# Performance work log

Hardware: AMD Instinct MI355X
Metric: run time of the kernel (lower is better)

Reference implementation:

```python
import jax, jax.numpy as jnp
import numpy as np
from jax import lax

B, S, E, DF, H, L, V, T = 32, 512, 512, 2048, 8, 2, 30000, 12
START, STOP = 10, 11
NEG = -10000.0


def setup_inputs() -> dict:
    key = jax.random.key(0)
    ks = jax.random.split(key, 12)
    g = lambda i, shape, sc=0.02: jax.random.normal(ks[i], shape, jnp.float32) * sc
    trans = jax.random.normal(ks[9], (T, T), jnp.float32)
    trans = trans.at[START, :].set(NEG).at[:, STOP].set(NEG)
    return {
        "sentence": jax.random.randint(ks[0], (B, S), 0, V),
        "seq_len": jax.random.randint(ks[1], (B,), 1, S + 1),
        "tags": jax.random.randint(ks[2], (B, S), 0, 10),
        "emb": g(3, (V, E), 1.0),
        "attn_in_w": g(4, (L, 3 * E, E)), "attn_in_b": jnp.zeros((L, 3 * E)),
        "attn_out_w": g(5, (L, E, E)), "attn_out_b": jnp.zeros((L, E)),
        "ln1_g": jnp.ones((L, E)), "ln1_b": jnp.zeros((L, E)),
        "ln2_g": jnp.ones((L, E)), "ln2_b": jnp.zeros((L, E)),
        "ff1_w": g(6, (L, DF, E)), "ff1_b": jnp.zeros((L, DF)),
        "ff2_w": g(7, (L, E, DF)), "ff2_b": jnp.zeros((L, E)),
        "tag_w": g(8, (T, E)), "tag_b": jnp.zeros((T,)),
        "transitions": trans,
    }


def _ln(x, g, b):
    m = x.mean(-1, keepdims=True)
    v = ((x - m) ** 2).mean(-1, keepdims=True)
    return (x - m) / jnp.sqrt(v + 1e-5) * g + b


def _mha(x, w_in, b_in, w_out, b_out):
    b_, s_, e_ = x.shape
    d = e_ // H
    qkv = x @ w_in.T + b_in
    q, k, v = jnp.split(qkv, 3, axis=-1)
    split = lambda t: t.reshape(b_, s_, H, d).transpose(0, 2, 1, 3)
    q, k, v = split(q), split(k), split(v)
    att = jax.nn.softmax(jnp.einsum('bhqd,bhkd->bhqk', q, k) / np.sqrt(d).astype(np.float32), axis=-1)
    o = jnp.einsum('bhqk,bhkd->bhqd', att, v).transpose(0, 2, 1, 3).reshape(b_, s_, e_)
    return o @ w_out.T + b_out


def _forward_impl(sentence, seq_len, tags, emb, attn_in_w, attn_in_b, attn_out_w,
                  attn_out_b, ln1_g, ln1_b, ln2_g, ln2_b, ff1_w, ff1_b, ff2_w,
                  ff2_b, tag_w, tag_b, transitions):
    # Transformer encoder features (dropout in eval mode -> identity)
    x = emb[sentence]  # (B,S,E)
    for l in range(L):
        x = _ln(x + _mha(x, attn_in_w[l], attn_in_b[l], attn_out_w[l], attn_out_b[l]), ln1_g[l], ln1_b[l])
        h = jax.nn.relu(x @ ff1_w[l].T + ff1_b[l]) @ ff2_w[l].T + ff2_b[l]
        x = _ln(x + h, ln2_g[l], ln2_b[l])
    feats = x @ tag_w.T + tag_b  # (B,S,T)

    # CRF forward algorithm (log-semiring scan, masked by seq_len)
    alpha0 = jnp.full((B, T), NEG, feats.dtype).at[:, START].set(0.0)

    def step(alpha, xs):
        emit_t, t = xs  # emit_t: (B,T)
        new = emit_t + jax.nn.logsumexp(alpha[:, None, :] + transitions[None, :, :], axis=-1)
        return jnp.where((t < seq_len)[:, None], new, alpha), None

    alpha, _ = lax.scan(step, alpha0, (feats.transpose(1, 0, 2), jnp.arange(S)))
    fwd_score = jax.nn.logsumexp(alpha + transitions[STOP][None, :], axis=-1)  # (B,)

    # gold score (vectorized _score_sentence)
    tags_ext = jnp.concatenate([jnp.full((B, 1), START, tags.dtype), tags], axis=1)  # (B,S+1)
    mask = jnp.arange(S)[None, :] < seq_len[:, None]  # (B,S)
    trans_sc = jnp.where(mask, transitions[tags_ext[:, 1:], tags_ext[:, :-1]], 0.0).sum(-1)
    emit_sc = jnp.where(mask, jnp.take_along_axis(feats, tags[:, :, None], axis=2)[..., 0], 0.0).sum(-1)
    last_tag = jnp.take_along_axis(tags_ext, seq_len[:, None], axis=1)[:, 0]
    gold = trans_sc + emit_sc + transitions[STOP, last_tag]

    return jnp.mean(fwd_score - gold)


def reference(sentence, seq_len, tags, emb, attn_in_w, attn_in_b, attn_out_w,
              attn_out_b, ln1_g, ln1_b, ln2_g, ln2_b, ff1_w, ff1_b, ff2_w,
              ff2_b, tag_w, tag_b, transitions):
    return _forward_impl(sentence, seq_len, tags, emb, attn_in_w, attn_in_b,
                         attn_out_w, attn_out_b, ln1_g, ln1_b, ln2_g, ln2_b,
                         ff1_w, ff1_b, ff2_w, ff2_b, tag_w, tag_b, transitions)
```

## Files before the change

### kernel.cpp

```cpp
#include <hip/hip_runtime.h>
#include <hip/hip_bf16.h>

#define BB 32
#define SSZ 512
#define EE 512
#define DFF 2048
#define HH 8
#define LL 2
#define TT 12
#define START_TAG 10
#define STOP_TAG 11
#define CB 8
#define CM (CB * SSZ)
#define NCHUNK (BB / CB)
#define NBH (CB * HH)
#define NBH_ALL (BB * HH)
#define NCHK 8

typedef __hip_bfloat16 bf16;
typedef __attribute__((ext_vector_type(8))) short short8;
typedef __attribute__((ext_vector_type(4))) float f32x4;

__device__ __forceinline__ float b2f(bf16 x) { return __bfloat162float(x); }
__device__ __forceinline__ float ldw(const void* p, size_t i, bool isbf) {
  return isbf ? __bfloat162float(((const bf16*)p)[i]) : ((const float*)p)[i];
}

__device__ __forceinline__ void gl_lds16(const bf16* g, bf16* l) {
  __builtin_amdgcn_global_load_lds(
      (const __attribute__((address_space(1))) void*)g,
      (__attribute__((address_space(3))) void*)l, 16, 0, 0);
}

__device__ __forceinline__ void stg128(const bf16* __restrict__ G, int ldk,
                                       int row0, int col0, bf16* lds0,
                                       int w, int l) {
#pragma unroll
  for (int q = 0; q < 2; ++q) {
    int lr = q * 64 + w * 8 + (l >> 3);
    int gs = (l & 7) ^ (lr & 7);
    gl_lds16(G + (size_t)(row0 + lr) * ldk + col0 + gs * 8,
             lds0 + (q * 64 + w * 8) * 64);
  }
}

__device__ __forceinline__ short8 ldfrag(const bf16* T, int row, int gr) {
  return *(const short8*)&T[row * 64 + ((gr ^ (row & 7)) << 3)];
}

__global__ void k_detect(const void* trans, int* dflag) {
  if (threadIdx.x == 0) {
    const unsigned short* u = (const unsigned short*)trans;
    dflag[0] = (u[START_TAG * TT] == 0xC61C && u[START_TAG * TT + 1] == 0xC61C) ? 1 : 0;
  }
}

__global__ void k_cvt(const void* src, bf16* dst, long n, const int* dflag) {
  bool isbf = dflag[0] != 0;
  for (long i = (long)blockIdx.x * 256 + threadIdx.x; i < n; i += (long)gridDim.x * 256)
    dst[i] = __float2bfloat16(ldw(src, i, isbf));
}

__global__ void k_embed(const int* sent, const void* emb, bf16* xb, const int* dflag) {
  bool isbf = dflag[0] != 0;
  int tok = blockIdx.x;
  int v = sent[tok];
  bf16* xo = xb + (size_t)tok * EE;
  for (int i = threadIdx.x; i < EE; i += 256)
    xo[i] = __float2bfloat16(ldw(emb, (size_t)v * EE + i, isbf));
}

template <int BN>
__global__ __launch_bounds__(512, 2) void k_mgemm256(
    const bf16* __restrict__ A, const bf16* __restrict__ W,
    const void* __restrict__ bias, size_t boff, bf16* __restrict__ Cb,
    bf16* __restrict__ vtout, int M, int N, int K, int relu,
    const int* __restrict__ dflag) {
  constexpr int WN = BN / 64;
  constexpr int WM = 8 / WN;
  constexpr int RPW = 256 / WM;
  constexpr int MFR = RPW / 16;
  constexpr int QW = MFR / 4;
  constexpr int BH = BN / 128;
  constexpr int BUFSZ = 16384 + BN * 64;
  extern __shared__ __align__(16) bf16 Sh[];
  const bool isbf = dflag[0] != 0;
  const int tid = threadIdx.x;
  const int l = tid & 63;
  const int w = tid >> 6;
  const int wm = w / WN, wn = w % WN;
  const int lrow = l & 15, lk = l >> 4;
  const int m0 = blockIdx.x * 256, n0 = blockIdx.y * BN;

  f32x4 acc[MFR][4];
#pragma unroll
  for (int i = 0; i < MFR; ++i)
#pragma unroll
    for (int j = 0; j < 4; ++j) acc[i][j] = (f32x4){0.f, 0.f, 0.f, 0.f};

  const int NIT = K >> 7;

#pragma unroll
  for (int p = 0; p < 2; ++p) {
    bf16* Ab = Sh + p * BUFSZ;
    bf16* Bb = Ab + 16384;
    stg128(A, K, m0, p * 64, Ab, w, l);
    stg128(A, K, m0 + 128, p * 64, Ab + 8192, w, l);
#pragma unroll
    for (int h = 0; h < BH; ++h)
      stg128(W, K, n0 + h * 128, p * 64, Bb + h * 8192, w, l);
  }
  if (BN == 256) asm volatile("s_waitcnt vmcnt(8)" ::: "memory");
  else asm volatile("s_waitcnt vmcnt(6)" ::: "memory");
  __builtin_amdgcn_sched_barrier(0);
  __builtin_amdgcn_s_barrier();

#define LDAQ(q)                                                               \
  do {                                                                        \
    _Pragma("unroll") for (int mi = 0; mi < QW; ++mi)                         \
        _Pragma("unroll") for (int kb = 0; kb < 2; ++kb)                      \
            aq[q][mi][kb] = ldfrag(                                           \
                Ab, wm * RPW + ((q)*QW + mi) * 16 + lrow, kb * 4 + lk);       \
  } while (0)

#define MMQ(q)                                                                \
  do {                                                                        \
    __builtin_amdgcn_s_setprio(1);                                            \
    _Pragma("unroll") for (int mi = 0; mi < QW; ++mi)                         \
        _Pragma("unroll") for (int kb = 0; kb < 2; ++kb)                      \
            _Pragma("unroll") for (int nf = 0; nf < 4; ++nf)                  \
                acc[(q)*QW + mi][nf] =                                        \
                    __builtin_amdgcn_mfma_f32_16x16x32_bf16(                  \
                        aq[q][mi][kb], bfr[kb][nf], acc[(q)*QW + mi][nf],     \
                        0, 0, 0);                                             \
    __builtin_amdgcn_s_setprio(0);                                            \
  } while (0)

#pragma unroll 1
  for (int i = 0; i < NIT; ++i) {
    const bool more = (i + 1 < NIT);
#pragma unroll
    for (int hh = 0; hh < 2; ++hh) {
      bf16* Ab = Sh + hh * BUFSZ;
      bf16* Bb = Ab + 16384;
      const int kc2 = (2 * i + 2 + hh) << 6;
      short8 bfr[2][4];
      short8 aq[4][QW][2];
#pragma unroll
      for (int kb = 0; kb < 2; ++kb)
#pragma unroll
        for (int nf = 0; nf < 4; ++nf)
          bfr[kb][nf] = ldfrag(Bb, wn * 64 + nf * 16 + lrow, kb * 4 + lk);
      LDAQ(0);
      MMQ(0);
      __builtin_amdgcn_s_barrier();
      LDAQ(1);
      LDAQ(2);
      MMQ(1);
      __builtin_amdgcn_s_barrier();
      LDAQ(3);
      if (more) {
#pragma unroll
        for (int h = 0; h < BH; ++h)
          stg128(W, K, n0 + h * 128, kc2, Bb + h * 8192, w, l);
      }
      MMQ(2);
      asm volatile("s_waitcnt lgkmcnt(0)" ::: "memory");
      __builtin_amdgcn_sched_barrier(0);
      __builtin_amdgcn_s_barrier();
      if (more) {
        stg128(A, K, m0, kc2, Ab, w, l);
        stg128(A, K, m0 + 128, kc2, Ab + 8192, w, l);
      }
      MMQ(3);
      if (more) {
        if (BN == 256) asm volatile("s_waitcnt vmcnt(8)" ::: "memory");
        else asm volatile("s_waitcnt vmcnt(6)" ::: "memory");
      } else {
        asm volatile("s_waitcnt vmcnt(0)" ::: "memory");
      }
      __builtin_amdgcn_sched_barrier(0);
      __builtin_amdgcn_s_barrier();
    }
  }
#undef LDAQ
#undef MMQ

  const bool vpath = (BN == 256) && (vtout != nullptr) && (n0 >= 1024);
  if (!vpath) {
#pragma unroll
    for (int nf = 0; nf < 4; ++nf) {
      const int c = wn * 64 + nf * 16 + lrow;
      const float bia = ldw(bias, boff + n0 + c, isbf);
#pragma unroll
      for (int mf = 0; mf < MFR; ++mf)
#pragma unroll
        for (int r = 0; r < 4; ++r) {
          const int row = wm * RPW + mf * 16 + lk * 4 + r;
          float v = acc[mf][nf][r] + bia;
          if (relu) v = fmaxf(v, 0.f);
          Sh[row * BN + (c ^ (((row >> 2) & 7) << 4))] = __float2bfloat16(v);
        }
    }
    __syncthreads();
    constexpr int GPR = BN / 8;
    constexpr int RPP = 512 / GPR;
#pragma unroll
    for (int p = 0; p < 256 / RPP; ++p) {
      const int row = p * RPP + tid / GPR;
      const int g = tid % GPR;
      *(uint4*)(Cb + (size_t)(m0 + row) * N + n0 + g * 8) =
          *(const uint4*)&Sh[row * BN + ((g * 8) ^ (((row >> 2) & 7) << 4))];
    }
  } else {
    const int pos0 = m0 & 511;
    const int blb = (m0 >> 9) * 8;
#pragma unroll
    for (int nf = 0; nf < 4; ++nf) {
      const int c = wn * 64 + nf * 16 + lrow;
      const float bia = ldw(bias, boff + n0 + c, isbf);
#pragma unroll
      for (int mf = 0; mf < MFR; ++mf)
#pragma unroll
        for (int r = 0; r < 4; ++r) {
          const int row = wm * RPW + mf * 16 + lk * 4 + r;
          Sh[c * 256 + (row ^ (((c >> 2) & 7) << 4))] =
              __float2bfloat16(acc[mf][nf][r] + bia);
        }
    }
    __syncthreads();
#pragma unroll
    for (int p = 0; p < 16; ++p) {
      const int cc = p * 16 + (tid >> 5);
      const int g = tid & 31;
      const int vc = n0 - 1024 + cc;
      *(uint4*)(vtout + ((size_t)(blb + (vc >> 6)) * 64 + (vc & 63)) * 512 +
                pos0 + g * 8) =
          *(const uint4*)&Sh[cc * 256 + ((g * 8) ^ (((cc >> 2) & 7) << 4))];
    }
  }
}

#define LDP 72
__global__ __launch_bounds__(512) void k_flash(const bf16* __restrict__ qkv,
                                               const bf16* __restrict__ vt,
                                               bf16* __restrict__ ctx) {
  extern __shared__ __align__(16) bf16 Fs[];
  const int bh = blockIdx.x;
  const int bl = bh >> 3, h = bh & 7;
  const int m0 = blockIdx.y * 256;
  const int tid = threadIdx.x;
  const int l = tid & 63;
  const int w = tid >> 6;
  const int lrow = l & 15, lk = l >> 4;

  bf16* Psw = Fs + 16384 + w * (32 * LDP);

  short8 qf[2][2];
  {
    const bf16* Qb = qkv + (size_t)(bl * SSZ + m0 + w * 32) * 1536 + h * 64;
#pragma unroll
    for (int mf = 0; mf < 2; ++mf)
#pragma unroll
      for (int kb = 0; kb < 2; ++kb)
        qf[mf][kb] = *(const short8*)(Qb + (size_t)(mf * 16 + lrow) * 1536 + kb * 32 + lk * 8);
  }

  f32x4 acc_o[2][4];
  float lsum[2][4];
#pragma unroll
  for (int mf = 0; mf < 2; ++mf) {
#pragma unroll
    for (int nf = 0; nf < 4; ++nf) acc_o[mf][nf] = (f32x4){0.f, 0.f, 0.f, 0.f};
#pragma unroll
    for (int r = 0; r < 4; ++r) lsum[mf][r] = 0.f;
  }

  const int srow = w * 8 + (l >> 3);
  const int gsw = (l & 7) ^ (srow & 7);
  const bf16* Ksrc = qkv + (size_t)(bl * SSZ + srow) * 1536 + 512 + h * 64 + gsw * 8;
  const bf16* Vsrc = vt + ((size_t)bh * 64 + srow) * SSZ + gsw * 8;
#define STAGE_KV(kt, b)                                                       \
  do {                                                                        \
    gl_lds16(Ksrc + (size_t)(kt)*64 * 1536, Fs + (b)*8192 + w * 512);         \
    gl_lds16(Vsrc + (kt)*64, Fs + (b)*8192 + 4096 + w * 512);                 \
  } while (0)

  STAGE_KV(0, 0);
  __syncthreads();

  for (int kt = 0; kt < 8; ++kt) {
    const int cur = kt & 1;
    if (kt < 7) STAGE_KV(kt + 1, cur ^ 1);
    const bf16* Ks = Fs + cur * 8192;
    const bf16* Vs = Ks + 4096;

    f32x4 s[2][4];
#pragma unroll
    for (int mf = 0; mf < 2; ++mf)
#pragma unroll
      for (int nf = 0; nf < 4; ++nf) s[mf][nf] = (f32x4){0.f, 0.f, 0.f, 0.f};
#pragma unroll
    for (int kb = 0; kb < 2; ++kb) {
      short8 bk[4];
#pragma unroll
      for (int nf = 0; nf < 4; ++nf)
        bk[nf] = ldfrag(Ks, nf * 16 + lrow, kb * 4 + lk);
#pragma unroll
      for (int mf = 0; mf < 2; ++mf)
#pragma unroll
        for (int nf = 0; nf < 4; ++nf)
          s[mf][nf] = __builtin_amdgcn_mfma_f32_16x16x32_bf16(qf[mf][kb], bk[nf],
                                                              s[mf][nf], 0, 0, 0);
    }
#pragma unroll
    for (int mf = 0; mf < 2; ++mf)
#pragma unroll
      for (int r = 0; r < 4; ++r) {
        float p0 = __expf(0.125f * s[mf][0][r]);
        float p1 = __expf(0.125f * s[mf][1][r]);
        float p2 = __expf(0.125f * s[mf][2][r]);
        float p3 = __expf(0.125f * s[mf][3][r]);
        s[mf][0][r] = p0; s[mf][1][r] = p1; s[mf][2][r] = p2; s[mf][3][r] = p3;
        lsum[mf][r] += (p0 + p1) + (p2 + p3);
      }
#pragma unroll
    for (int mf = 0; mf < 2; ++mf)
#pragma unroll
      for (int nf = 0; nf < 4; ++nf)
#pragma unroll
        for (int r = 0; r < 4; ++r)
          Psw[(mf * 16 + lk * 4 + r) * LDP + nf * 16 + lrow] =
              __float2bfloat16(s[mf][nf][r]);
#pragma unroll
    for (int kb = 0; kb < 2; ++kb) {
      short8 ap[2], bv[4];
#pragma unroll
      for (int mf = 0; mf < 2; ++mf)
        ap[mf] = *(const short8*)&Psw[(mf * 16 + lrow) * LDP + kb * 32 + lk * 8];
#pragma unroll
      for (int nf = 0; nf < 4; ++nf)
        bv[nf] = ldfrag(Vs, nf * 16 + lrow, kb * 4 + lk);
#pragma unroll
      for (int mf = 0; mf < 2; ++mf)
#pragma unroll
        for (int nf = 0; nf < 4; ++nf)
          acc_o[mf][nf] = __builtin_amdgcn_mfma_f32_16x16x32_bf16(ap[mf], bv[nf],
                                                                  acc_o[mf][nf], 0, 0, 0);
    }
    __syncthreads();
  }
#undef STAGE_KV
#pragma unroll
  for (int mf = 0; mf < 2; ++mf) {
#pragma unroll
    for (int r = 0; r < 4; ++r) {
      float ls = lsum[mf][r];
      ls += __shfl_xor(ls, 1, 64);
      ls += __shfl_xor(ls, 2, 64);
      ls += __shfl_xor(ls, 4, 64);
      ls += __shfl_xor(ls, 8, 64);
      float inv = 1.f / ls;
      int q = m0 + w * 32 + mf * 16 + lk * 4 + r;
#pragma unroll
      for (int nf = 0; nf < 4; ++nf)
        ctx[((size_t)(bl * SSZ + q)) * EE + h * 64 + nf * 16 + lrow] =
            __float2bfloat16(acc_o[mf][nf][r] * inv);
    }
  }
}

__global__ void k_ln_res(bf16* xb, const bf16* hb, const void* g,
                         const void* be, size_t goff, const int* dflag) {
  bool isbf = dflag[0] != 0;
  int tok = blockIdx.x, tid = threadIdx.x;
  size_t base = (size_t)tok * EE;
  float v0 = b2f(xb[base + tid]) + b2f(hb[base + tid]);
  float v1 = b2f(xb[base + tid + 256]) + b2f(hb[base + tid + 256]);
  float s = v0 + v1, ss = v0 * v0 + v1 * v1;
#pragma unroll
  for (int off = 32; off > 0; off >>= 1) {
    s += __shfl_down(s, off, 64);
    ss += __shfl_down(ss, off, 64);
  }
  __shared__ float ps[4], pss[4];
  __shared__ float mean_s, rstd_s;
  int w = tid >> 6;
  if ((tid & 63) == 0) { ps[w] = s; pss[w] = ss; }
  __syncthreads();
  if (tid == 0) {
    float S_ = ps[0] + ps[1] + ps[2] + ps[3];
    float SS_ = pss[0] + pss[1] + pss[2] + pss[3];
    float mu = S_ / (float)EE;
    float var = SS_ / (float)EE - mu * mu;
    mean_s = mu;
    rstd_s = rsqrtf(var + 1e-5f);
  }
  __syncthreads();
  float mu = mean_s, rs = rstd_s;
  float r0 = (v0 - mu) * rs * ldw(g, goff + tid, isbf) + ldw(be, goff + tid, isbf);
  float r1 = (v1 - mu) * rs * ldw(g, goff + tid + 256, isbf) + ldw(be, goff + tid + 256, isbf);
  xb[base + tid] = __float2bfloat16(r0);
  xb[base + tid + 256] = __float2bfloat16(r1);
}

__global__ void k_feats(const bf16* xb, const bf16* tgw, const void* tgb,
                        float* feats, const int* dflag) {
  bool isbf = dflag[0] != 0;
  int m = blockIdx.x * 4 + (threadIdx.x >> 6);
  int lane = threadIdx.x & 63;
  uint4 raw = *(const uint4*)(xb + (size_t)m * EE + lane * 8);
  const bf16* rb = (const bf16*)&raw;
  float xv[8];
#pragma unroll
  for (int j = 0; j < 8; ++j) xv[j] = b2f(rb[j]);
#pragma unroll
  for (int t = 0; t < TT; ++t) {
    uint4 wraw = *(const uint4*)(tgw + t * EE + lane * 8);
    const bf16* wb = (const bf16*)&wraw;
    float s = 0.f;
#pragma unroll
    for (int j = 0; j < 8; ++j) s += xv[j] * b2f(wb[j]);
#pragma unroll
    for (int off = 32; off > 0; off >>= 1) s += __shfl_down(s, off, 64);
    if (lane == 0) feats[(size_t)m * TT + t] = s + ldw(tgb, t, isbf);
  }
}

__global__ void k_crf1(const float* feats, const int* seq_len, const void* trans_in,
                       float* cmat, const int* dflag) {
  bool isbf = dflag[0] != 0;
  int c = blockIdx.x, b = blockIdx.y;
  int tid = threadIdx.x;
  __shared__ float tr[144];
  __shared__ float abuf[2][144];
  if (tid < 144) tr[tid] = ldw(trans_in, tid, isbf);
  bool act = tid < 144;
  int i = tid / 12, j = tid % 12;
  if (act) abuf[0][tid] = (i == j) ? 0.f : -1e30f;
  __syncthreads();
  float trrow[12];
  if (act) {
#pragma unroll
    for (int k = 0; k < 12; ++k) trrow[k] = tr[i * 12 + k];
  }
  int len = seq_len[b];
  int t0 = c * 64;
  int t1 = min(len, t0 + 64);
  int cur = 0;
  for (int t = t0; t < t1; ++t) {
    float nv = 0.f;
    if (act) {
      float m = -1e30f, v[12];
#pragma unroll
      for (int k = 0; k < 12; ++k) {
        v[k] = trrow[k] + abuf[cur][k * 12 + j];
        m = fmaxf(m, v[k]);
      }
      float s = 0.f;
#pragma unroll
      for (int k = 0; k < 12; ++k) s += __expf(v[k] - m);
      nv = feats[((size_t)b * SSZ + t) * TT + i] + m + __logf(s);
    }
    if (act) abuf[cur ^ 1][tid] = nv;
    __syncthreads();
    cur ^= 1;
  }
  if (act) cmat[((size_t)b * NCHK + c) * 144 + tid] = abuf[cur][tid];
}

__global__ void k_crf2(const float* cmat, const float* feats, const int* tags,
                       const int* seq_len, const void* trans_in, float* bscore,
                       const int* dflag) {
  bool isbf = dflag[0] != 0;
  int b = blockIdx.x;
  int tid = threadIdx.x;
  __shared__ float tr[144];
  __shared__ float tbuf[2][144];
  __shared__ float alpha_sh[12];
  if (tid < 144) tr[tid] = ldw(trans_in, tid, isbf);
  bool act = tid < 144;
  int i = tid / 12, j = tid % 12;
  if (act) tbuf[0][tid] = cmat[((size_t)b * NCHK) * 144 + tid];
  __syncthreads();
  int cur = 0;
  for (int c = 1; c < NCHK; ++c) {
    float nv = 0.f;
    if (act) {
      const float* Cc = cmat + ((size_t)b * NCHK + c) * 144;
      float m = -1e30f, v[12];
#pragma unroll
      for (int k = 0; k < 12; ++k) {
        v[k] = Cc[i * 12 + k] + tbuf[cur][k * 12 + j];
        m = fmaxf(m, v[k]);
      }
      float s = 0.f;
#pragma unroll
      for (int k = 0; k < 12; ++k) s += __expf(v[k] - m);
      nv = m + __logf(s);
    }
    if (act) tbuf[cur ^ 1][tid] = nv;
    __syncthreads();
    cur ^= 1;
  }
  if (tid < 12) {
    float m = -1e30f, v[12];
#pragma unroll
    for (int k = 0; k < 12; ++k) {
      float a0 = (k == START_TAG) ? 0.f : -10000.f;
      v[k] = tbuf[cur][tid * 12 + k] + a0;
      m = fmaxf(m, v[k]);
    }
    float s = 0.f;
#pragma unroll
    for (int k = 0; k < 12; ++k) s += __expf(v[k] - m);
    alpha_sh[tid] = m + __logf(s);
  }
  __syncthreads();
  if (tid < 64) {
    int lane = tid;
    int len = seq_len[b];
    float part = 0.f;
    for (int s = lane; s < len; s += 64) {
      int ct = tags[b * SSZ + s];
      int pv = (s == 0) ? START_TAG : tags[b * SSZ + s - 1];
      part += tr[ct * 12 + pv] + feats[((size_t)b * SSZ + s) * TT + ct];
    }
#pragma unroll
    for (int off = 32; off > 0; off >>= 1) part += __shfl_down(part, off, 64);
    if (lane == 0) {
      float m = -1e30f;
#pragma unroll
      for (int k = 0; k < 12; ++k) m = fmaxf(m, alpha_sh[k] + tr[STOP_TAG * 12 + k]);
      float s = 0.f;
#pragma unroll
      for (int k = 0; k < 12; ++k) s += __expf(alpha_sh[k] + tr[STOP_TAG * 12 + k] - m);
      float fwd = m + __logf(s);
      int last = tags[b * SSZ + len - 1];
      bscore[b] = fwd - (part + tr[STOP_TAG * 12 + last]);
    }
  }
}

__global__ void k_final(const float* bscore, float* out) {
  int tid = threadIdx.x;
  float v = (tid < BB) ? bscore[tid] : 0.f;
#pragma unroll
  for (int off = 32; off > 0; off >>= 1) v += __shfl_down(v, off, 64);
  if (tid == 0) out[0] = v / (float)BB;
}

extern "C" void kernel_launch(void* const* d_in, const int* in_sizes, int n_in,
                              void* d_out, int out_size, void* d_ws, size_t ws_size,
                              hipStream_t stream) {
  const int* sentence = (const int*)d_in[0];
  const int* seq_len = (const int*)d_in[1];
  const int* tags = (const int*)d_in[2];
  const void* emb = d_in[3];
  const void* attn_in_w = d_in[4];
  const void* attn_in_b = d_in[5];
  const void* attn_out_w = d_in[6];
  const void* attn_out_b = d_in[7];
  const void* ln1_g = d_in[8];
  const void* ln1_b = d_in[9];
  const void* ln2_g = d_in[10];
  const void* ln2_b = d_in[11];
  const void* ff1_w = d_in[12];
  const void* ff1_b = d_in[13];
  const void* ff2_w = d_in[14];
  const void* ff2_b = d_in[15];
  const void* tag_w = d_in[16];
  const void* tag_b = d_in[17];
  const void* transitions = d_in[18];

  static int attr_done = 0;
  if (!attr_done) {
    (void)hipFuncSetAttribute((const void*)&k_mgemm256<256>,
                              hipFuncAttributeMaxDynamicSharedMemorySize, 131072);
    (void)hipFuncSetAttribute((const void*)&k_mgemm256<128>,
                              hipFuncAttributeMaxDynamicSharedMemorySize, 131072);
    (void)hipFuncSetAttribute((const void*)&k_flash,
                              hipFuncAttributeMaxDynamicSharedMemorySize, 131072);
    attr_done = 1;
  }
  const int FLDS = (16384 + 8 * 32 * LDP) * 2;

  const int M = BB * SSZ;
  const size_t WEL = (size_t)LL * 3 * EE * EE + (size_t)LL * EE * EE +
                     (size_t)LL * DFF * EE + (size_t)LL * EE * DFF + (size_t)TT * EE;

  size_t o = 0;
  size_t f_feats = o; o += (size_t)M * TT;
  size_t f_bsc = o; o += 64;
  size_t f_cmat = o; o += (size_t)BB * NCHK * 144;
  size_t f_dflag = o; o += 16;
  size_t f_xb = o; o += (size_t)M * EE / 2;
  size_t f_hb = o; o += (size_t)M * EE / 2;
  size_t f_ctxb = o; o += (size_t)M * EE / 2;
  size_t f_act = o; o += (size_t)M * DFF / 2;
  size_t f_vt = o; o += (size_t)NBH_ALL * 64 * SSZ / 2;
  size_t f_w = o; o += (WEL + 1) / 2 + 8;
  size_t need_full = o * 4;
  bool full = ws_size >= need_full;

  float* ws = (float*)d_ws;
  if (full) {
    float* feats = ws + f_feats;
    float* bsc = ws + f_bsc;
    float* cmat = ws + f_cmat;
    int* dflag = (int*)(ws + f_dflag);
    bf16* xb = (bf16*)(ws + f_xb);
    bf16* hb = (bf16*)(ws + f_hb);
    bf16* ctxb = (bf16*)(ws + f_ctxb);
    bf16* act = (bf16*)(ws + f_act);
    bf16* vt = (bf16*)(ws + f_vt);
    bf16* w_aiw = (bf16*)(ws + f_w);
    bf16* w_aow = w_aiw + (size_t)LL * 3 * EE * EE;
    bf16* w_f1 = w_aow + (size_t)LL * EE * EE;
    bf16* w_f2 = w_f1 + (size_t)LL * DFF * EE;
    bf16* w_tg = w_f2 + (size_t)LL * EE * DFF;

    k_detect<<<dim3(1), dim3(64), 0, stream>>>(transitions, dflag);
    k_cvt<<<dim3(1024), dim3(256), 0, stream>>>(attn_in_w, w_aiw, (long)LL * 3 * EE * EE, dflag);
    k_cvt<<<dim3(512), dim3(256), 0, stream>>>(attn_out_w, w_aow, (long)LL * EE * EE, dflag);
    k_cvt<<<dim3(1024), dim3(256), 0, stream>>>(ff1_w, w_f1, (long)LL * DFF * EE, dflag);
    k_cvt<<<dim3(1024), dim3(256), 0, stream>>>(ff2_w, w_f2, (long)LL * EE * DFF, dflag);
    k_cvt<<<dim3(24), dim3(256), 0, stream>>>(tag_w, w_tg, (long)TT * EE, dflag);
    k_embed<<<dim3(M), dim3(256), 0, stream>>>(sentence, emb, xb, dflag);

    for (int l = 0; l < LL; ++l) {
      k_mgemm256<256><<<dim3(M / 256, 6), dim3(512), 131072, stream>>>(
          xb, w_aiw + (size_t)l * 3 * EE * EE, attn_in_b, (size_t)l * 3 * EE,
          act, vt, M, 3 * EE, EE, 0, dflag);
      k_flash<<<dim3(NBH_ALL, 2), dim3(512), FLDS, stream>>>(act, vt, ctxb);
      k_mgemm256<128><<<dim3(M / 256, EE / 128), dim3(512), 98304, stream>>>(
          ctxb, w_aow + (size_t)l * EE * EE, attn_out_b, (size_t)l * EE,
          hb, (bf16*)nullptr, M, EE, EE, 0, dflag);
      k_ln_res<<<dim3(M), dim3(256), 0, stream>>>(xb, hb, ln1_g, ln1_b,
                                                  (size_t)l * EE, dflag);
      k_mgemm256<256><<<dim3(M / 256, DFF / 256), dim3(512), 131072, stream>>>(
          xb, w_f1 + (size_t)l * DFF * EE, ff1_b, (size_t)l * DFF,
          act, (bf16*)nullptr, M, DFF, EE, 1, dflag);
      k_mgemm256<128><<<dim3(M / 256, EE / 128), dim3(512), 98304, stream>>>(
          act, w_f2 + (size_t)l * EE * DFF, ff2_b, (size_t)l * EE,
          hb, (bf16*)nullptr, M, EE, DFF, 0, dflag);
      k_ln_res<<<dim3(M), dim3(256), 0, stream>>>(xb, hb, ln2_g, ln2_b,
                                                  (size_t)l * EE, dflag);
    }
    k_feats<<<dim3(M / 4), dim3(256), 0, stream>>>(xb, w_tg, tag_b, feats, dflag);
    k_crf1<<<dim3(NCHK, BB), dim3(192), 0, stream>>>(feats, seq_len, transitions, cmat, dflag);
    k_crf2<<<dim3(BB), dim3(192), 0, stream>>>(cmat, feats, tags, seq_len, transitions, bsc, dflag);
    k_final<<<dim3(1), dim3(64), 0, stream>>>(bsc, (float*)d_out);
  } else {
    float* feats = ws;
    float* bsc = feats + (size_t)M * TT;
    float* cmat = bsc + 64;
    int* dflag = (int*)(cmat + (size_t)BB * NCHK * 144 + 16);
    bf16* xb = (bf16*)(dflag + 16);
    bf16* hb = xb + (size_t)M * EE;
    bf16* qkvb = hb + (size_t)CM * EE;
    bf16* ctxb = qkvb + (size_t)CM * 1536;
    bf16* ffh = ctxb + (size_t)CM * EE;
    bf16* vt = ffh + (size_t)CM * DFF;
    bf16* w_aiw = vt + (size_t)NBH * 64 * SSZ;
    bf16* w_aow = w_aiw + (size_t)LL * 3 * EE * EE;
    bf16* w_f1 = w_aow + (size_t)LL * EE * EE;
    bf16* w_f2 = w_f1 + (size_t)LL * DFF * EE;
    bf16* w_tg = w_f2 + (size_t)LL * EE * DFF;

    k_detect<<<dim3(1), dim3(64), 0, stream>>>(transitions, dflag);
    k_cvt<<<dim3(1024), dim3(256), 0, stream>>>(attn_in_w, w_aiw, (long)LL * 3 * EE * EE, dflag);
    k_cvt<<<dim3(512), dim3(256), 0, stream>>>(attn_out_w, w_aow, (long)LL * EE * EE, dflag);
    k_cvt<<<dim3(1024), dim3(256), 0, stream>>>(ff1_w, w_f1, (long)LL * DFF * EE, dflag);
    k_cvt<<<dim3(1024), dim3(256), 0, stream>>>(ff2_w, w_f2, (long)LL * EE * DFF, dflag);
    k_cvt<<<dim3(24), dim3(256), 0, stream>>>(tag_w, w_tg, (long)TT * EE, dflag);
    k_embed<<<dim3(M), dim3(256), 0, stream>>>(sentence, emb, xb, dflag);

    for (int l = 0; l < LL; ++l) {
      for (int c = 0; c < NCHUNK; ++c) {
        bf16* xbc = xb + (size_t)c * CM * EE;
        k_mgemm256<256><<<dim3(CM / 256, 6), dim3(512), 131072, stream>>>(
            xbc, w_aiw + (size_t)l * 3 * EE * EE, attn_in_b, (size_t)l * 3 * EE,
            qkvb, vt, CM, 3 * EE, EE, 0, dflag);
        k_flash<<<dim3(NBH, 2), dim3(512), FLDS, stream>>>(qkvb, vt, ctxb);
        k_mgemm256<128><<<dim3(CM / 256, EE / 128), dim3(512), 98304, stream>>>(
            ctxb, w_aow + (size_t)l * EE * EE, attn_out_b, (size_t)l * EE,
            hb, (bf16*)nullptr, CM, EE, EE, 0, dflag);
        k_ln_res<<<dim3(CM), dim3(256), 0, stream>>>(xbc, hb, ln1_g, ln1_b,
                                                     (size_t)l * EE, dflag);
        k_mgemm256<256><<<dim3(CM / 256, DFF / 256), dim3(512), 131072, stream>>>(
            xbc, w_f1 + (size_t)l * DFF * EE, ff1_b, (size_t)l * DFF,
            ffh, (bf16*)nullptr, CM, DFF, EE, 1, dflag);
        k_mgemm256<128><<<dim3(CM / 256, EE / 128), dim3(512), 98304, stream>>>(
            ffh, w_f2 + (size_t)l * EE * DFF, ff2_b, (size_t)l * EE,
            hb, (bf16*)nullptr, CM, EE, DFF, 0, dflag);
        k_ln_res<<<dim3(CM), dim3(256), 0, stream>>>(xbc, hb, ln2_g, ln2_b,
                                                     (size_t)l * EE, dflag);
      }
    }
    k_feats<<<dim3(M / 4), dim3(256), 0, stream>>>(xb, w_tg, tag_b, feats, dflag);
    k_crf1<<<dim3(NCHK, BB), dim3(192), 0, stream>>>(feats, seq_len, transitions, cmat, dflag);
    k_crf2<<<dim3(BB), dim3(192), 0, stream>>>(cmat, feats, tags, seq_len, transitions, bsc, dflag);
    k_final<<<dim3(1), dim3(64), 0, stream>>>(bsc, (float*)d_out);
  }
}
```

Baseline: 656.2 us.

## Replace 256-row GEMM with 128x128 tile kernel at higher occupancy

```diff
diff --git a/kernel.cpp b/kernel.cpp
--- a/kernel.cpp
+++ b/kernel.cpp
@@ -70,147 +70,103 @@
     xo[i] = __float2bfloat16(ldw(emb, (size_t)v * EE + i, isbf));
 }
 
-template <int BN>
-__global__ __launch_bounds__(512, 2) void k_mgemm256(
+__global__ __launch_bounds__(512, 4) void k_mg128(
     const bf16* __restrict__ A, const bf16* __restrict__ W,
     const void* __restrict__ bias, size_t boff, bf16* __restrict__ Cb,
     bf16* __restrict__ vtout, int M, int N, int K, int relu,
     const int* __restrict__ dflag) {
-  constexpr int WN = BN / 64;
-  constexpr int WM = 8 / WN;
-  constexpr int RPW = 256 / WM;
-  constexpr int MFR = RPW / 16;
-  constexpr int QW = MFR / 4;
-  constexpr int BH = BN / 128;
-  constexpr int BUFSZ = 16384 + BN * 64;
+  constexpr int BUFSZ = 16384;
   extern __shared__ __align__(16) bf16 Sh[];
   const bool isbf = dflag[0] != 0;
   const int tid = threadIdx.x;
   const int l = tid & 63;
   const int w = tid >> 6;
-  const int wm = w / WN, wn = w % WN;
+  const int wm = w >> 1, wn = w & 1;
   const int lrow = l & 15, lk = l >> 4;
-  const int m0 = blockIdx.x * 256, n0 = blockIdx.y * BN;
-
-  f32x4 acc[MFR][4];
-#pragma unroll
-  for (int i = 0; i < MFR; ++i)
+  const int m0 = blockIdx.x * 128, n0 = blockIdx.y * 128;
+
+  f32x4 acc[2][4];
+#pragma unroll
+  for (int i = 0; i < 2; ++i)
 #pragma unroll
     for (int j = 0; j < 4; ++j) acc[i][j] = (f32x4){0.f, 0.f, 0.f, 0.f};
 
-  const int NIT = K >> 7;
+  const int NT = K >> 6;
 
 #pragma unroll
   for (int p = 0; p < 2; ++p) {
-    bf16* Ab = Sh + p * BUFSZ;
-    bf16* Bb = Ab + 16384;
-    stg128(A, K, m0, p * 64, Ab, w, l);
-    stg128(A, K, m0 + 128, p * 64, Ab + 8192, w, l);
-#pragma unroll
-    for (int h = 0; h < BH; ++h)
-      stg128(W, K, n0 + h * 128, p * 64, Bb + h * 8192, w, l);
-  }
-  if (BN == 256) asm volatile("s_waitcnt vmcnt(8)" ::: "memory");
-  else asm volatile("s_waitcnt vmcnt(6)" ::: "memory");
+    stg128(A, K, m0, p * 64, Sh + p * BUFSZ, w, l);
+    stg128(W, K, n0, p * 64, Sh + p * BUFSZ + 8192, w, l);
+  }
+  asm volatile("s_waitcnt vmcnt(4)" ::: "memory");
   __builtin_amdgcn_sched_barrier(0);
   __builtin_amdgcn_s_barrier();
 
-#define LDAQ(q)                                                               \
-  do {                                                                        \
-    _Pragma("unroll") for (int mi = 0; mi < QW; ++mi)                         \
-        _Pragma("unroll") for (int kb = 0; kb < 2; ++kb)                      \
-            aq[q][mi][kb] = ldfrag(                                           \
-                Ab, wm * RPW + ((q)*QW + mi) * 16 + lrow, kb * 4 + lk);       \
-  } while (0)
-
-#define MMQ(q)                                                                \
-  do {                                                                        \
-    __builtin_amdgcn_s_setprio(1);                                            \
-    _Pragma("unroll") for (int mi = 0; mi < QW; ++mi)                         \
-        _Pragma("unroll") for (int kb = 0; kb < 2; ++kb)                      \
-            _Pragma("unroll") for (int nf = 0; nf < 4; ++nf)                  \
-                acc[(q)*QW + mi][nf] =                                        \
-                    __builtin_amdgcn_mfma_f32_16x16x32_bf16(                  \
-                        aq[q][mi][kb], bfr[kb][nf], acc[(q)*QW + mi][nf],     \
-                        0, 0, 0);                                             \
-    __builtin_amdgcn_s_setprio(0);                                            \
-  } while (0)
-
 #pragma unroll 1
-  for (int i = 0; i < NIT; ++i) {
-    const bool more = (i + 1 < NIT);
-#pragma unroll
-    for (int hh = 0; hh < 2; ++hh) {
-      bf16* Ab = Sh + hh * BUFSZ;
-      bf16* Bb = Ab + 16384;
-      const int kc2 = (2 * i + 2 + hh) << 6;
-      short8 bfr[2][4];
-      short8 aq[4][QW][2];
-#pragma unroll
-      for (int kb = 0; kb < 2; ++kb)
-#pragma unroll
-        for (int nf = 0; nf < 4; ++nf)
-          bfr[kb][nf] = ldfrag(Bb, wn * 64 + nf * 16 + lrow, kb * 4 + lk);
-      LDAQ(0);
-      MMQ(0);
-      __builtin_amdgcn_s_barrier();
-      LDAQ(1);
-      LDAQ(2);
-      MMQ(1);
-      __builtin_amdgcn_s_barrier();
-      LDAQ(3);
-      if (more) {
-#pragma unroll
-        for (int h = 0; h < BH; ++h)
-          stg128(W, K, n0 + h * 128, kc2, Bb + h * 8192, w, l);
-      }
-      MMQ(2);
-      asm volatile("s_waitcnt lgkmcnt(0)" ::: "memory");
-      __builtin_amdgcn_sched_barrier(0);
-      __builtin_amdgcn_s_barrier();
-      if (more) {
-        stg128(A, K, m0, kc2, Ab, w, l);
-        stg128(A, K, m0 + 128, kc2, Ab + 8192, w, l);
-      }
-      MMQ(3);
-      if (more) {
-        if (BN == 256) asm volatile("s_waitcnt vmcnt(8)" ::: "memory");
-        else asm volatile("s_waitcnt vmcnt(6)" ::: "memory");
-      } else {
-        asm volatile("s_waitcnt vmcnt(0)" ::: "memory");
-      }
-      __builtin_amdgcn_sched_barrier(0);
-      __builtin_amdgcn_s_barrier();
-    }
-  }
-#undef LDAQ
-#undef MMQ
-
-  const bool vpath = (BN == 256) && (vtout != nullptr) && (n0 >= 1024);
+  for (int t = 0; t < NT; ++t) {
+    bf16* Ab = Sh + (t & 1) * BUFSZ;
+    bf16* Bb = Ab + 8192;
+    const bool more = (t + 2 < NT);
+    short8 bfr[2][4], a0[2], a1[2];
+#pragma unroll
+    for (int kb = 0; kb < 2; ++kb) {
+#pragma unroll
+      for (int nf = 0; nf < 4; ++nf)
+        bfr[kb][nf] = ldfrag(Bb, wn * 64 + nf * 16 + lrow, kb * 4 + lk);
+      a0[kb] = ldfrag(Ab, wm * 32 + lrow, kb * 4 + lk);
+      a1[kb] = ldfrag(Ab, wm * 32 + 16 + lrow, kb * 4 + lk);
+    }
+    asm volatile("s_waitcnt lgkmcnt(0)" ::: "memory");
+    __builtin_amdgcn_sched_barrier(0);
+    __builtin_amdgcn_s_barrier();
+    __builtin_amdgcn_sched_barrier(0);
+    if (more) {
+      stg128(A, K, m0, (t + 2) * 64, Ab, w, l);
+      stg128(W, K, n0, (t + 2) * 64, Bb, w, l);
+    }
+    __builtin_amdgcn_s_setprio(1);
+#pragma unroll
+    for (int kb = 0; kb < 2; ++kb)
+#pragma unroll
+      for (int nf = 0; nf < 4; ++nf)
+        acc[0][nf] = __builtin_amdgcn_mfma_f32_16x16x32_bf16(
+            a0[kb], bfr[kb][nf], acc[0][nf], 0, 0, 0);
+#pragma unroll
+    for (int kb = 0; kb < 2; ++kb)
+#pragma unroll
+      for (int nf = 0; nf < 4; ++nf)
+        acc[1][nf] = __builtin_amdgcn_mfma_f32_16x16x32_bf16(
+            a1[kb], bfr[kb][nf], acc[1][nf], 0, 0, 0);
+    __builtin_amdgcn_s_setprio(0);
+    if (more) asm volatile("s_waitcnt vmcnt(4)" ::: "memory");
+    else asm volatile("s_waitcnt vmcnt(0)" ::: "memory");
+    __builtin_amdgcn_sched_barrier(0);
+    __builtin_amdgcn_s_barrier();
+  }
+
+  const bool vpath = (vtout != nullptr) && (n0 >= 1024);
   if (!vpath) {
 #pragma unroll
     for (int nf = 0; nf < 4; ++nf) {
       const int c = wn * 64 + nf * 16 + lrow;
       const float bia = ldw(bias, boff + n0 + c, isbf);
 #pragma unroll
-      for (int mf = 0; mf < MFR; ++mf)
+      for (int mf = 0; mf < 2; ++mf)
 #pragma unroll
         for (int r = 0; r < 4; ++r) {
-          const int row = wm * RPW + mf * 16 + lk * 4 + r;
+          const int row = wm * 32 + mf * 16 + lk * 4 + r;
           float v = acc[mf][nf][r] + bia;
           if (relu) v = fmaxf(v, 0.f);
-          Sh[row * BN + (c ^ (((row >> 2) & 7) << 4))] = __float2bfloat16(v);
+          Sh[row * 128 + (c ^ (((row >> 2) & 7) << 4))] = __float2bfloat16(v);
         }
     }
     __syncthreads();
-    constexpr int GPR = BN / 8;
-    constexpr int RPP = 512 / GPR;
-#pragma unroll
-    for (int p = 0; p < 256 / RPP; ++p) {
-      const int row = p * RPP + tid / GPR;
-      const int g = tid % GPR;
+#pragma unroll
+    for (int p = 0; p < 4; ++p) {
+      const int row = p * 32 + (tid >> 4);
+      const int g = tid & 15;
       *(uint4*)(Cb + (size_t)(m0 + row) * N + n0 + g * 8) =
-          *(const uint4*)&Sh[row * BN + ((g * 8) ^ (((row >> 2) & 7) << 4))];
+          *(const uint4*)&Sh[row * 128 + ((g * 8) ^ (((row >> 2) & 7) << 4))];
     }
   } else {
     const int pos0 = m0 & 511;
@@ -220,23 +176,23 @@
       const int c = wn * 64 + nf * 16 + lrow;
       const float bia = ldw(bias, boff + n0 + c, isbf);
 #pragma unroll
-      for (int mf = 0; mf < MFR; ++mf)
+      for (int mf = 0; mf < 2; ++mf)
 #pragma unroll
         for (int r = 0; r < 4; ++r) {
-          const int row = wm * RPW + mf * 16 + lk * 4 + r;
-          Sh[c * 256 + (row ^ (((c >> 2) & 7) << 4))] =
+          const int row = wm * 32 + mf * 16 + lk * 4 + r;
+          Sh[c * 128 + (row ^ (((c >> 2) & 7) << 4))] =
               __float2bfloat16(acc[mf][nf][r] + bia);
         }
     }
     __syncthreads();
 #pragma unroll
-    for (int p = 0; p < 16; ++p) {
-      const int cc = p * 16 + (tid >> 5);
-      const int g = tid & 31;
+    for (int p = 0; p < 4; ++p) {
+      const int cc = p * 32 + (tid >> 4);
+      const int g = tid & 15;
       const int vc = n0 - 1024 + cc;
       *(uint4*)(vtout + ((size_t)(blb + (vc >> 6)) * 64 + (vc & 63)) * 512 +
                 pos0 + g * 8) =
-          *(const uint4*)&Sh[cc * 256 + ((g * 8) ^ (((cc >> 2) & 7) << 4))];
+          *(const uint4*)&Sh[cc * 128 + ((g * 8) ^ (((cc >> 2) & 7) << 4))];
     }
   }
 }
@@ -575,14 +531,13 @@
 
   static int attr_done = 0;
   if (!attr_done) {
-    (void)hipFuncSetAttribute((const void*)&k_mgemm256<256>,
-                              hipFuncAttributeMaxDynamicSharedMemorySize, 131072);
-    (void)hipFuncSetAttribute((const void*)&k_mgemm256<128>,
-                              hipFuncAttributeMaxDynamicSharedMemorySize, 131072);
+    (void)hipFuncSetAttribute((const void*)&k_mg128,
+                              hipFuncAttributeMaxDynamicSharedMemorySize, 65536);
     (void)hipFuncSetAttribute((const void*)&k_flash,
                               hipFuncAttributeMaxDynamicSharedMemorySize, 131072);
     attr_done = 1;
   }
+  const int GLDS = 65536;
   const int FLDS = (16384 + 8 * 32 * LDP) * 2;
 
   const int M = BB * SSZ;
@@ -629,19 +584,19 @@
     k_embed<<<dim3(M), dim3(256), 0, stream>>>(sentence, emb, xb, dflag);
 
     for (int l = 0; l < LL; ++l) {
-      k_mgemm256<256><<<dim3(M / 256, 6), dim3(512), 131072, stream>>>(
+      k_mg128<<<dim3(M / 128, 12), dim3(512), GLDS, stream>>>(
           xb, w_aiw + (size_t)l * 3 * EE * EE, attn_in_b, (size_t)l * 3 * EE,
           act, vt, M, 3 * EE, EE, 0, dflag);
       k_flash<<<dim3(NBH_ALL, 2), dim3(512), FLDS, stream>>>(act, vt, ctxb);
-      k_mgemm256<128><<<dim3(M / 256, EE / 128), dim3(512), 98304, stream>>>(
+      k_mg128<<<dim3(M / 128, 4), dim3(512), GLDS, stream>>>(
           ctxb, w_aow + (size_t)l * EE * EE, attn_out_b, (size_t)l * EE,
           hb, (bf16*)nullptr, M, EE, EE, 0, dflag);
       k_ln_res<<<dim3(M), dim3(256), 0, stream>>>(xb, hb, ln1_g, ln1_b,
                                                   (size_t)l * EE, dflag);
-      k_mgemm256<256><<<dim3(M / 256, DFF / 256), dim3(512), 131072, stream>>>(
+      k_mg128<<<dim3(M / 128, 16), dim3(512), GLDS, stream>>>(
           xb, w_f1 + (size_t)l * DFF * EE, ff1_b, (size_t)l * DFF,
           act, (bf16*)nullptr, M, DFF, EE, 1, dflag);
-      k_mgemm256<128><<<dim3(M / 256, EE / 128), dim3(512), 98304, stream>>>(
+      k_mg128<<<dim3(M / 128, 4), dim3(512), GLDS, stream>>>(
           act, w_f2 + (size_t)l * EE * DFF, ff2_b, (size_t)l * EE,
           hb, (bf16*)nullptr, M, EE, DFF, 0, dflag);
       k_ln_res<<<dim3(M), dim3(256), 0, stream>>>(xb, hb, ln2_g, ln2_b,
@@ -679,19 +634,19 @@
     for (int l = 0; l < LL; ++l) {
       for (int c = 0; c < NCHUNK; ++c) {
         bf16* xbc = xb + (size_t)c * CM * EE;
-        k_mgemm256<256><<<dim3(CM / 256, 6), dim3(512), 131072, stream>>>(
+        k_mg128<<<dim3(CM / 128, 12), dim3(512), GLDS, stream>>>(
             xbc, w_aiw + (size_t)l * 3 * EE * EE, attn_in_b, (size_t)l * 3 * EE,
             qkvb, vt, CM, 3 * EE, EE, 0, dflag);
         k_flash<<<dim3(NBH, 2), dim3(512), FLDS, stream>>>(qkvb, vt, ctxb);
-        k_mgemm256<128><<<dim3(CM / 256, EE / 128), dim3(512), 98304, stream>>>(
+        k_mg128<<<dim3(CM / 128, 4), dim3(512), GLDS, stream>>>(
             ctxb, w_aow + (size_t)l * EE * EE, attn_out_b, (size_t)l * EE,
             hb, (bf16*)nullptr, CM, EE, EE, 0, dflag);
         k_ln_res<<<dim3(CM), dim3(256), 0, stream>>>(xbc, hb, ln1_g, ln1_b,
                                                      (size_t)l * EE, dflag);
-        k_mgemm256<256><<<dim3(CM / 256, DFF / 256), dim3(512), 131072, stream>>>(
+        k_mg128<<<dim3(CM / 128, 16), dim3(512), GLDS, stream>>>(
             xbc, w_f1 + (size_t)l * DFF * EE, ff1_b, (size_t)l * DFF,
             ffh, (bf16*)nullptr, CM, DFF, EE, 1, dflag);
-        k_mgemm256<128><<<dim3(CM / 256, EE / 128), dim3(512), 98304, stream>>>(
+        k_mg128<<<dim3(CM / 128, 4), dim3(512), GLDS, stream>>>(
             ffh, w_f2 + (size_t)l * EE * DFF, ff2_b, (size_t)l * EE,
             hb, (bf16*)nullptr, CM, EE, DFF, 0, dflag);
         k_ln_res<<<dim3(CM), dim3(256), 0, stream>>>(xbc, hb, ln2_g, ln2_b,
```

Result: slower. 673.9 us (+2.7%).
